# Optimization experiments

Hardware: AMD Instinct MI355X
Metric: run time of the kernel (lower is better)

## Reference

```python
import jax, jax.numpy as jnp
import numpy as np

QS, B, C, H, M = 512, 8, 1024, 16, 1536
HC = C // H
KS = QS  # xk = xv = xq (self-attention)


def setup_inputs() -> dict:
    key = jax.random.key(0)
    ks = jax.random.split(key, 16)
    scale = 1.0 / np.sqrt(C)
    xq = jax.random.normal(ks[0], (QS, B, C), jnp.float32)
    memory_kv = jax.random.normal(ks[1], (M, B, H, 2 * HC), jnp.float32)
    memory_length = jax.random.randint(ks[2], (B,), 0, M)
    pad = jax.random.randint(ks[3], (B,), 0, KS)
    mask = jnp.zeros((QS, KS, B), dtype=bool)
    Wq = jax.random.normal(ks[4], (C, C), jnp.float32) * scale
    bq = jax.random.normal(ks[5], (C,), jnp.float32) * 0.02
    Wk = jax.random.normal(ks[6], (C, C), jnp.float32) * scale
    bk = jax.random.normal(ks[7], (C,), jnp.float32) * 0.02
    Wv = jax.random.normal(ks[8], (C, C), jnp.float32) * scale
    bv = jax.random.normal(ks[9], (C,), jnp.float32) * 0.02
    Wo = jax.random.normal(ks[10], (C, C), jnp.float32) * scale
    bo = jax.random.normal(ks[11], (C,), jnp.float32) * 0.02
    return dict(xq=xq, pad=pad, mask=mask, memory_length=memory_length,
                memory_kv=memory_kv, Wq=Wq, bq=bq, Wk=Wk, bk=bk,
                Wv=Wv, bv=bv, Wo=Wo, bo=bo)


def _memory_attention(xq, pad, mask, memory_length, memory_kv,
                      Wq, bq, Wk, bk, Wv, bv, Wo, bo):
    qs, b, c = xq.shape
    m = memory_kv.shape[0]
    T = m + KS  # combined kv length (static upper bound = max(memory_length)+pad)

    # qkv projections (torch Linear: x @ W.T + b), layout (seq, batch, h, hc)
    q = (xq @ Wq.T + bq).reshape(qs, b, H, HC)
    k = (xq @ Wk.T + bk).reshape(KS, b, H, HC)
    v = (xq @ Wv.T + bv).reshape(KS, b, H, HC)

    # cat_padded_seqs as a static-shape gather: slot t of batch i is
    #   memory[t]        if t <  memory_length[i]
    #   new[t - len_i]   if t - len_i < pad[i]
    #   padding (masked) otherwise
    t = jnp.arange(T)[:, None]                      # [T,1]
    L = memory_length[None, :]                      # [1,b]
    in_mem = t < L                                  # [T,b]
    off = t - L                                     # [T,b] offset into new seq
    in_new = (off >= 0) & (off < pad[None, :])      # [T,b]
    idx_new = jnp.clip(off, 0, KS - 1)              # [T,b]

    mem_k = memory_kv[..., :HC]
    mem_v = memory_kv[..., HC:]
    mem_idx = jnp.minimum(jnp.arange(T), m - 1)     # [T]
    k_mem = mem_k[mem_idx]                          # [T,b,H,HC]
    v_mem = mem_v[mem_idx]

    gidx = jnp.broadcast_to(idx_new[:, :, None, None], (T, b, H, HC))
    k_new = jnp.take_along_axis(k, gidx, axis=0)    # [T,b,H,HC]
    v_new = jnp.take_along_axis(v, gidx, axis=0)

    sel = in_mem[:, :, None, None]
    k_comb = jnp.where(sel, k_mem, k_new)
    v_comb = jnp.where(sel, v_mem, v_new)

    # combined padding/user mask, True = masked out
    midx = jnp.broadcast_to(idx_new[None, :, :], (qs, T, b))
    user_m = jnp.take_along_axis(mask, midx, axis=1)        # [qs,T,b]
    comb_mask = jnp.where(in_mem[None], False,
                          jnp.where(in_new[None], user_m, True))

    # attention
    temperature = 1.0 / np.sqrt(HC)
    a = jnp.einsum('sbhc,tbhc->stbh', q, k_comb) * temperature
    a = jnp.where(comb_mask[:, :, :, None], -jnp.inf, a)
    p = jax.nn.softmax(a, axis=1)
    p = jnp.nan_to_num(p)  # fully-masked rows -> 0 (matches torch)
    x = jnp.einsum('stbh,tbhc->sbhc', p, v_comb).reshape(qs, b, c)
    return x @ Wo.T + bo


def reference(xq, pad, mask, memory_length, memory_kv,
              Wq, bq, Wk, bk, Wv, bv, Wo, bo):
    return _memory_attention(xq, pad, mask, memory_length, memory_kv,
                             Wq, bq, Wk, bk, Wv, bv, Wo, bo)
```

## Files before the change

### kernel.cpp

```cpp
#include <hip/hip_runtime.h>

#define QS_ 512
#define B_  8
#define C_  1024
#define H_  16
#define HC_ 64
#define M_  1536
#define KS_ 512
#define TMX 2048

typedef __attribute__((ext_vector_type(8))) short bf16x8;
typedef __attribute__((ext_vector_type(4))) float f32x4;

__device__ __forceinline__ short f2bf(float f) {
    unsigned u = __float_as_uint(f);
    unsigned r = (u + 0x7FFF + ((u >> 16) & 1)) >> 16;
    return (short)r;
}

__device__ __forceinline__ void gload_lds16(const void* g, void* l) {
    __builtin_amdgcn_global_load_lds(
        (const __attribute__((address_space(1))) unsigned int*)g,
        (__attribute__((address_space(3))) unsigned int*)l, 16, 0, 0);
}

__global__ __launch_bounds__(256) void prep_all(
    const float* __restrict__ xq,
    const float* __restrict__ w0, const float* __restrict__ w1,
    const float* __restrict__ w2, const float* __restrict__ w3,
    short* __restrict__ xqb,
    short* __restrict__ d0, short* __restrict__ d1,
    short* __restrict__ d2, short* __restrict__ d3,
    const float* __restrict__ mkv, short* __restrict__ kall,
    short* __restrict__ vall,
    const unsigned char* __restrict__ maskb, const int* __restrict__ mlen,
    const int* __restrict__ padv, unsigned char* __restrict__ mbits)
{
    __shared__ short T[64][72];
    const int bx = blockIdx.x;
    const int tid = threadIdx.x;

    if (bx < 4096) {
        int idx = bx * 256 + tid;
        const float* src; short* dst; int i;
        if (idx < 524288) { src = xq; dst = xqb; i = idx; }
        else {
            int sel = (idx >> 17) & 3;
            i = idx & 131071;
            src = sel == 0 ? w0 : sel == 1 ? w1 : sel == 2 ? w2 : w3;
            dst = sel == 0 ? d0 : sel == 1 ? d1 : sel == 2 ? d2 : d3;
        }
        const float4* s = (const float4*)src + (size_t)i * 2;
        float4 a = s[0], bq = s[1];
        short o[8];
        o[0] = f2bf(a.x);  o[1] = f2bf(a.y);  o[2] = f2bf(a.z);  o[3] = f2bf(a.w);
        o[4] = f2bf(bq.x); o[5] = f2bf(bq.y); o[6] = f2bf(bq.z); o[7] = f2bf(bq.w);
        *(uint4*)(dst + (size_t)i * 8) = *(uint4*)o;
        return;
    }

    if (bx < 7168) {
        const int idx = bx - 4096;
        const int tc = idx % 24;
        const int h  = (idx / 24) & 15;
        const int b  = idx / 384;
        const int row = tid >> 2, part = tid & 3;
        const int t = tc * 64 + row;
        const int g = b * H_ + h;
        const float4* src = (const float4*)(mkv + (((size_t)t * B_ + b) * H_ + h) * 128 + part * 32);
        short o[32];
#pragma unroll
        for (int j = 0; j < 8; ++j) {
            float4 f = src[j];
            o[j * 4 + 0] = f2bf(f.x); o[j * 4 + 1] = f2bf(f.y);
            o[j * 4 + 2] = f2bf(f.z); o[j * 4 + 3] = f2bf(f.w);
        }
        if (part < 2) {
            short* d = kall + ((size_t)g * TMX + t) * 64 + part * 32;
#pragma unroll
            for (int j = 0; j < 4; ++j) ((uint4*)d)[j] = ((uint4*)o)[j];
        } else {
            int hc0 = (part - 2) * 32;
#pragma unroll
            for (int j = 0; j < 32; ++j) T[hc0 + j][row] = o[j];
        }
        __syncthreads();
        const int hc = tid >> 2, seg = tid & 3;
        uint4 a = *(const uint4*)&T[hc][seg * 16];
        uint4 c = *(const uint4*)&T[hc][seg * 16 + 8];
        short* d = vall + ((size_t)g * HC_ + hc) * TMX + tc * 64 + seg * 16;
        ((uint4*)d)[0] = a; ((uint4*)d)[1] = c;
        return;
    }

    if (bx < 7296) {
        const int i = bx - 7168;
        const int b = i >> 4, h = i & 15;
        const int L = mlen[b], P = padv[b];
        const int te = L + P;
        const int z0 = max(1536, L + 512);
        const int z1 = min(2048, (te + 63) & ~63);
        if (z1 > z0) {
            const int g = b * 16 + h;
            const int hc = tid >> 2;
            short* rowp = vall + ((size_t)g * HC_ + hc) * TMX;
            for (int c = z0 + (tid & 3); c < z1; c += 4) rowp[c] = 0;
        }
        return;
    }

    {
        const int j = bx - 7296;
        const int b = j >> 6;
        const int q = (j & 63) * 8 + (tid >> 5);
        const int wordIdx = tid & 31;
        const int L = mlen[b], P = padv[b];
        const int tb = wordIdx * 64;
        unsigned long long w;
        if (tb + 63 < L) {
            w = 0ull;
        } else if (tb >= L + P) {
            w = ~0ull;
        } else {
            w = 0ull;
            const unsigned char* mq = maskb + (size_t)q * (KS_ * B_) + b;
#pragma unroll 4
            for (int k = 0; k < 64; ++k) {
                int t = tb + k;
                int bit;
                if (t < L) bit = 0;
                else {
                    int off = t - L;
                    bit = (off >= P) ? 1 : (mq[(size_t)off * B_] ? 1 : 0);
                }
                w |= (unsigned long long)bit << k;
            }
        }
        ((unsigned long long*)mbits)[(((size_t)(b * 512 + q)) << 5) + wordIdx] = w;
    }
}

template <bool BF16OUT, bool KSC>
__device__ __forceinline__ void gemm128_body(
    short (*As)[64], short (*Ws)[64],
    const short* __restrict__ A, const short* __restrict__ W,
    const float* __restrict__ bias, void* __restrict__ outv,
    int n0, int j0, float oscale, const int* __restrict__ mlen)
{
    const int tid  = threadIdx.x;
    const int lane = tid & 63;
    const int wave = tid >> 6;
    const int wm = (wave & 1) * 64;
    const int wn = (wave >> 1) * 64;
    const int lr = lane & 15;
    const int quad = lane >> 4;

    f32x4 acc[4][4];
#pragma unroll
    for (int i = 0; i < 4; ++i)
#pragma unroll
        for (int j = 0; j < 4; ++j)
            acc[i][j] = (f32x4){0.f, 0.f, 0.f, 0.f};

    for (int k0 = 0; k0 < C_; k0 += 64) {
#pragma unroll
        for (int p = 0; p < 4; ++p) {
            int flat = p * 256 + tid;
            int r = flat >> 3, c8 = (flat & 7) * 8;
            gload_lds16(A + (size_t)(n0 + r) * C_ + k0 + c8, (short*)As + flat * 8);
        }
#pragma unroll
        for (int p = 0; p < 4; ++p) {
            int flat = p * 256 + tid;
            int r = flat >> 3, c8 = (flat & 7) * 8;
            gload_lds16(W + (size_t)(j0 + r) * C_ + k0 + c8, (short*)Ws + flat * 8);
        }
        __syncthreads();
#pragma unroll
        for (int ks = 0; ks < 2; ++ks) {
            const int kk = ks * 32 + quad * 8;
            bf16x8 afrag[4], bfrag[4];
#pragma unroll
            for (int im = 0; im < 4; ++im)
                afrag[im] = *(const bf16x8*)&As[wm + im * 16 + lr][kk];
#pragma unroll
            for (int jn = 0; jn < 4; ++jn)
                bfrag[jn] = *(const bf16x8*)&Ws[wn + jn * 16 + lr][kk];
#pragma unroll
            for (int im = 0; im < 4; ++im)
#pragma unroll
                for (int jn = 0; jn < 4; ++jn)
                    acc[im][jn] = __builtin_amdgcn_mfma_f32_16x16x32_bf16(
                        afrag[im], bfrag[jn], acc[im][jn], 0, 0, 0);
        }
        __syncthreads();
    }

    if constexpr (KSC) {
        int ml[8];
#pragma unroll
        for (int i = 0; i < 8; ++i) ml[i] = mlen[i];
#pragma unroll
        for (int jn = 0; jn < 4; ++jn) {
            const int col = j0 + wn + jn * 16 + lr;
            const int h = col >> 6, hc = col & 63;
            const float bv = bias[col];
#pragma unroll
            for (int im = 0; im < 4; ++im) {
                const int row = n0 + wm + im * 16 + quad * 4;
#pragma unroll
                for (int r = 0; r < 4; ++r) {
                    const int rr = row + r;
                    const int s = rr >> 3, b = rr & 7;
                    float v = acc[im][jn][r] + bv;
                    ((short*)outv)[((size_t)((b * 16 + h) * TMX) + ml[b] + s) * 64 + hc] = f2bf(v);
                }
            }
        }
    } else {
#pragma unroll
        for (int jn = 0; jn < 4; ++jn) {
            const int col = j0 + wn + jn * 16 + lr;
            const float bv = bias[col];
#pragma unroll
            for (int im = 0; im < 4; ++im) {
                const int row = n0 + wm + im * 16 + quad * 4;
#pragma unroll
                for (int r = 0; r < 4; ++r) {
                    float v = (acc[im][jn][r] + bv) * oscale;
                    if (BF16OUT)
                        ((short*)outv)[(size_t)(row + r) * C_ + col] = f2bf(v);
                    else
                        ((float*)outv)[(size_t)(row + r) * C_ + col] = v;
                }
            }
        }
    }
}

template <bool BF16OUT>
__global__ __launch_bounds__(256) void gemm128(
    const short* __restrict__ A, const short* __restrict__ W,
    const float* __restrict__ bias, void* __restrict__ outv)
{
    __shared__ short As[128][64];
    __shared__ short Ws[128][64];
    gemm128_body<BF16OUT, false>(As, Ws, A, W, bias, outv,
                                 blockIdx.x * 128, blockIdx.y * 128, 1.0f, nullptr);
}

__global__ __launch_bounds__(256) void gemm128_qkv(
    const short* __restrict__ A,
    const short* __restrict__ Wq, const short* __restrict__ Wk,
    const short* __restrict__ Wv,
    const float* __restrict__ bq, const float* __restrict__ bk,
    const float* __restrict__ bv,
    short* __restrict__ oq, short* __restrict__ kall, short* __restrict__ ov,
    const int* __restrict__ mlen)
{
    __shared__ short As[128][64];
    __shared__ short Ws[128][64];
    const int sel = blockIdx.y >> 3;
    const int n0 = blockIdx.x * 128;
    const int j0 = (blockIdx.y & 7) * 128;
    if (sel == 0)
        gemm128_body<true, false>(As, Ws, A, Wq, bq, oq, n0, j0, 0.125f, nullptr);
    else if (sel == 1)
        gemm128_body<true, true>(As, Ws, A, Wk, bk, kall, n0, j0, 1.0f, mlen);
    else
        gemm128_body<true, false>(As, Ws, A, Wv, bv, ov, n0, j0, 1.0f, nullptr);
}

__global__ __launch_bounds__(256) void scatter_kv(
    const short* __restrict__ vbuf, const int* __restrict__ mlen,
    short* __restrict__ vall)
{
    __shared__ short T[64][72];
    const int bx = blockIdx.x;
    const int tid = threadIdx.x;
    const int sc = bx & 7, h = (bx >> 3) & 15, b = bx >> 7;
    const int r = tid >> 2, seg = tid & 3;
    const int s = sc * 64 + r;
    const short* src = vbuf + ((size_t)s * B_ + b) * C_ + h * HC_ + seg * 16;
    short tmp[16];
    *(uint4*)&tmp[0] = ((const uint4*)src)[0];
    *(uint4*)&tmp[8] = ((const uint4*)src)[1];
#pragma unroll
    for (int j = 0; j < 16; ++j) T[seg * 16 + j][r] = tmp[j];
    __syncthreads();
    const int L = mlen[b];
    const int hc = tid >> 2;
    const int g = b * H_ + h;
    short* drow = vall + ((size_t)g * HC_ + hc) * TMX + L + sc * 64 + seg * 16;
    const short* srow = &T[hc][seg * 16];
#pragma unroll
    for (int j = 0; j < 16; ++j) drow[j] = srow[j];
}

__global__ __launch_bounds__(256, 4) void attn_block(
    const short* __restrict__ qb, const short* __restrict__ kall,
    const short* __restrict__ vall, const unsigned char* __restrict__ mbits,
    const int* __restrict__ mlen, const int* __restrict__ padv,
    short* __restrict__ xout)
{
    __shared__ short Ks[2][64][64];
    __shared__ short Vs[2][64][64];

    const int tid  = threadIdx.x;
    const int lane = tid & 63;
    const int wave = tid >> 6;
    const int lr   = lane & 15;
    const int quad = lane >> 4;
    const int bx = blockIdx.x;
    const int g  = ((bx >> 6) << 3) | (bx & 7);
    const int qg = (bx >> 3) & 7;
    const int b  = g >> 4, h = g & 15;
    const int tend = mlen[b] + padv[b];
    const float NEG = -1e30f;

    const int q = qg * 64 + wave * 16 + lr;

    const short* qrow = qb + ((size_t)q * B_ + b) * C_ + h * HC_;
    bf16x8 q0 = *(const bf16x8*)(qrow + quad * 8);
    bf16x8 q1 = *(const bf16x8*)(qrow + 32 + quad * 8);

    const char* kg = (const char*)(kall + (size_t)g * TMX * 64);
    const char* vg = (const char*)(vall + (size_t)g * HC_ * TMX);
    const unsigned char* mrow = mbits + ((size_t)(b * 512 + q) << 8);

    f32x4 O[4];
#pragma unroll
    for (int i = 0; i < 4; ++i) O[i] = (f32x4){0.f, 0.f, 0.f, 0.f};
    float mr = NEG, lsum = 0.f;

    const int nch = (tend + 63) >> 6;

    auto stage = [&](int t0, int buf) {
        char* KsB = (char*)Ks[buf];
        char* VsB = (char*)Vs[buf];
#pragma unroll
        for (int i = 0; i < 4; ++i) {
            int p = wave * 4 + i;
            int f = ((p & 7) << 6) + lane;
            int row = f >> 3;
            int c = ((f & 7) << 4) ^ ((row & 7) << 4);
            if (p < 8)
                gload_lds16(kg + (size_t)(t0 + row) * 128 + c,
                            KsB + (size_t)f * 16);
            else
                gload_lds16(vg + (size_t)row * (TMX * 2) + (size_t)t0 * 2 + c,
                            VsB + (size_t)f * 16);
        }
    };

    if (nch > 0) stage(0, 0);
    __syncthreads();

    int cur = 0;
    for (int ci = 0; ci < nch; ++ci) {
        const int t0 = ci << 6;

        unsigned long long mw = *(const unsigned long long*)(mrow + (t0 >> 3));

        if (ci + 1 < nch) stage((ci + 1) << 6, cur ^ 1);

        const char* KsB = (const char*)Ks[cur];
        const char* VsB = (const char*)Vs[cur];

        bf16x8 kf[4][2];
#pragma unroll
        for (int tt = 0; tt < 4; ++tt) {
            int t = tt * 16 + lr;
            int sw = (t & 7) << 4;
            kf[tt][0] = *(const bf16x8*)(KsB + t * 128 + ((quad * 16) ^ sw));
            kf[tt][1] = *(const bf16x8*)(KsB + t * 128 + ((64 + quad * 16) ^ sw));
        }

        __builtin_amdgcn_s_setprio(1);
        f32x4 S[4];
#pragma unroll
        for (int tt = 0; tt < 4; ++tt) {
            f32x4 z = (f32x4){0.f, 0.f, 0.f, 0.f};
            z = __builtin_amdgcn_mfma_f32_16x16x32_bf16(kf[tt][0], q0, z, 0, 0, 0);
            S[tt] = __builtin_amdgcn_mfma_f32_16x16x32_bf16(kf[tt][1], q1, z, 0, 0, 0);
        }
        __builtin_amdgcn_s_setprio(0);

        bf16x8 vf[4][2];
#pragma unroll
        for (int ht = 0; ht < 4; ++ht) {
            int hc = ht * 16 + lr;
            int sw = (hc & 7) << 4;
            vf[ht][0] = *(const bf16x8*)(VsB + hc * 128 + ((quad * 16) ^ sw));
            vf[ht][1] = *(const bf16x8*)(VsB + hc * 128 + ((64 + quad * 16) ^ sw));
        }

        float p4[4][4];
#pragma unroll
        for (int tt = 0; tt < 4; ++tt) {
            unsigned m4 = ((unsigned)(mw >> (tt * 16 + quad * 4))) & 15u;
#pragma unroll
            for (int r = 0; r < 4; ++r)
                p4[tt][r] = (m4 & (1u << r)) ? NEG : S[tt][r];
        }

        float rm = NEG;
#pragma unroll
        for (int tt = 0; tt < 4; ++tt)
#pragma unroll
            for (int r = 0; r < 4; ++r) rm = fmaxf(rm, p4[tt][r]);
        rm = fmaxf(rm, __shfl_xor(rm, 16, 64));
        rm = fmaxf(rm, __shfl_xor(rm, 32, 64));
        const float nm = fmaxf(fmaxf(mr, rm), -1e20f);
        const float al = __expf(mr - nm);
        float rs = 0.f;
#pragma unroll
        for (int tt = 0; tt < 4; ++tt)
#pragma unroll
            for (int r = 0; r < 4; ++r) {
                float e = __expf(p4[tt][r] - nm);
                p4[tt][r] = e;
                rs += e;
            }
        rs += __shfl_xor(rs, 16, 64);
        rs += __shfl_xor(rs, 32, 64);
        lsum = lsum * al + rs;
        mr = nm;
#pragma unroll
        for (int ht = 0; ht < 4; ++ht)
#pragma unroll
            for (int r = 0; r < 4; ++r) O[ht][r] *= al;

        bf16x8 pf[2];
        const int slA = ((quad & 1) * 2) * 16 + lr;
        const int slB = slA + 16;
        const unsigned sel = (quad & 2) ? 0x07060302u : 0x05040100u;
#pragma unroll
        for (int hf = 0; hf < 2; ++hf) {
            const int tt0 = hf * 2;
            unsigned pk[4];
#pragma unroll
            for (int r = 0; r < 4; ++r) {
                unsigned o;
                asm("v_cvt_pk_bf16_f32 %0, %1, %2"
                    : "=v"(o) : "v"(p4[tt0][r]), "v"(p4[tt0 + 1][r]));
                pk[r] = o;
            }
            unsigned uA[4], uB[4];
#pragma unroll
            for (int r = 0; r < 4; ++r) {
                uA[r] = (unsigned)__shfl((int)pk[r], slA, 64);
                uB[r] = (unsigned)__shfl((int)pk[r], slB, 64);
            }
            unsigned wv[4];
            wv[0] = __builtin_amdgcn_perm(uA[1], uA[0], sel);
            wv[1] = __builtin_amdgcn_perm(uA[3], uA[2], sel);
            wv[2] = __builtin_amdgcn_perm(uB[1], uB[0], sel);
            wv[3] = __builtin_amdgcn_perm(uB[3], uB[2], sel);
            pf[hf] = *(const bf16x8*)wv;
        }

        __builtin_amdgcn_s_setprio(1);
#pragma unroll
        for (int ht = 0; ht < 4; ++ht) {
            O[ht] = __builtin_amdgcn_mfma_f32_16x16x32_bf16(vf[ht][0], pf[0], O[ht], 0, 0, 0);
            O[ht] = __builtin_amdgcn_mfma_f32_16x16x32_bf16(vf[ht][1], pf[1], O[ht], 0, 0, 0);
        }
        __builtin_amdgcn_s_setprio(0);

        __syncthreads();
        cur ^= 1;
    }

    float inv = (lsum > 0.f) ? 1.0f / lsum : 0.f;
#pragma unroll
    for (int ht = 0; ht < 4; ++ht) {
        short ov[4];
#pragma unroll
        for (int r = 0; r < 4; ++r) ov[r] = f2bf(O[ht][r] * inv);
        short* d = xout + ((size_t)q * B_ + b) * C_ + h * HC_ + ht * 16 + quad * 4;
        *(long long*)d = *(const long long*)ov;
    }
}

extern "C" void kernel_launch(void* const* d_in, const int* in_sizes, int n_in,
                              void* d_out, int out_size, void* d_ws, size_t ws_size,
                              hipStream_t stream)
{
    const float* xq   = (const float*)d_in[0];
    const int*   pad  = (const int*)d_in[1];
    const unsigned char* maskb = (const unsigned char*)d_in[2];
    const int*   mlen = (const int*)d_in[3];
    const float* mkv  = (const float*)d_in[4];
    const float* Wq   = (const float*)d_in[5];
    const float* bq   = (const float*)d_in[6];
    const float* Wk   = (const float*)d_in[7];
    const float* bk   = (const float*)d_in[8];
    const float* Wv   = (const float*)d_in[9];
    const float* bv   = (const float*)d_in[10];
    const float* Wo   = (const float*)d_in[11];
    const float* bo   = (const float*)d_in[12];
    float* out = (float*)d_out;

    short* xqb  = (short*)d_ws;
    short* wqb  = xqb  + (size_t)4194304;
    short* wkb  = wqb  + (size_t)1048576;
    short* wvb  = wkb  + (size_t)1048576;
    short* wob  = wvb  + (size_t)1048576;
    short* kall = wob  + (size_t)1048576;
    short* vall = kall + (size_t)128 * TMX * 64;
    short* qbuf = vall + (size_t)128 * HC_ * TMX;
    short* vbuf = qbuf + (size_t)4194304;
    short* xbuf = vbuf + (size_t)4194304;
    unsigned char* mbits = (unsigned char*)(xbuf + (size_t)4194304);

    dim3 gblk(256);
    prep_all<<<dim3(7808), gblk, 0, stream>>>(
        xq, Wq, Wk, Wv, Wo, xqb, wqb, wkb, wvb, wob,
        mkv, kall, vall, maskb, mlen, pad, mbits);

    gemm128_qkv<<<dim3(32, 24), gblk, 0, stream>>>(
        xqb, wqb, wkb, wvb, bq, bk, bv, qbuf, kall, vbuf, mlen);

    scatter_kv<<<dim3(1024), gblk, 0, stream>>>(vbuf, mlen, vall);

    attn_block<<<dim3(1024), gblk, 0, stream>>>(qbuf, kall, vall, mbits,
                                                mlen, pad, xbuf);

    gemm128<false><<<dim3(32, 8), gblk, 0, stream>>>(xbuf, wob, bo, out);
}
```

Baseline: 345.8 us.

## Fuse V transpose-scatter into QKV GEMM epilogue and skip unused memory rows

The QKV GEMM's V branch now writes its output directly in the transposed, memory-length-offset layout the attention kernel reads. This removes the separate scatter_kv kernel and the intermediate vbuf round trip. The prep kernel also skips converting memory_kv tiles past each batch's used length, and skips loading rows that the new K/V will overwrite. In exchange, the V epilogue issues scattered 2-byte stores with a large stride, which may coalesce poorly.

```diff
diff --git a/kernel.cpp b/kernel.cpp
--- a/kernel.cpp
+++ b/kernel.cpp
@@ -64,21 +64,32 @@
         const int tc = idx % 24;
         const int h  = (idx / 24) & 15;
         const int b  = idx / 384;
+        const int L = mlen[b];
+        const int tendb = L + padv[b];
+        if (tc * 64 >= tendb) return;
         const int row = tid >> 2, part = tid & 3;
         const int t = tc * 64 + row;
         const int g = b * H_ + h;
-        const float4* src = (const float4*)(mkv + (((size_t)t * B_ + b) * H_ + h) * 128 + part * 32);
+        const bool skiprow = (t >= L) && (t < L + 512);
         short o[32];
-#pragma unroll
-        for (int j = 0; j < 8; ++j) {
-            float4 f = src[j];
-            o[j * 4 + 0] = f2bf(f.x); o[j * 4 + 1] = f2bf(f.y);
-            o[j * 4 + 2] = f2bf(f.z); o[j * 4 + 3] = f2bf(f.w);
+        if (!skiprow) {
+            const float4* src = (const float4*)(mkv + (((size_t)t * B_ + b) * H_ + h) * 128 + part * 32);
+#pragma unroll
+            for (int j = 0; j < 8; ++j) {
+                float4 f = src[j];
+                o[j * 4 + 0] = f2bf(f.x); o[j * 4 + 1] = f2bf(f.y);
+                o[j * 4 + 2] = f2bf(f.z); o[j * 4 + 3] = f2bf(f.w);
+            }
+        } else {
+#pragma unroll
+            for (int j = 0; j < 32; ++j) o[j] = 0;
         }
         if (part < 2) {
-            short* d = kall + ((size_t)g * TMX + t) * 64 + part * 32;
-#pragma unroll
-            for (int j = 0; j < 4; ++j) ((uint4*)d)[j] = ((uint4*)o)[j];
+            if (!skiprow) {
+                short* d = kall + ((size_t)g * TMX + t) * 64 + part * 32;
+#pragma unroll
+                for (int j = 0; j < 4; ++j) ((uint4*)d)[j] = ((uint4*)o)[j];
+            }
         } else {
             int hc0 = (part - 2) * 32;
 #pragma unroll
@@ -140,7 +151,7 @@
     }
 }
 
-template <bool BF16OUT, bool KSC>
+template <int EPI>
 __device__ __forceinline__ void gemm128_body(
     short (*As)[64], short (*Ws)[64],
     const short* __restrict__ A, const short* __restrict__ W,
@@ -196,7 +207,7 @@
         __syncthreads();
     }
 
-    if constexpr (KSC) {
+    if constexpr (EPI == 2 || EPI == 3) {
         int ml[8];
 #pragma unroll
         for (int i = 0; i < 8; ++i) ml[i] = mlen[i];
@@ -213,7 +224,10 @@
                     const int rr = row + r;
                     const int s = rr >> 3, b = rr & 7;
                     float v = acc[im][jn][r] + bv;
-                    ((short*)outv)[((size_t)((b * 16 + h) * TMX) + ml[b] + s) * 64 + hc] = f2bf(v);
+                    if (EPI == 2)
+                        ((short*)outv)[((size_t)((b * 16 + h) * TMX) + ml[b] + s) * 64 + hc] = f2bf(v);
+                    else
+                        ((short*)outv)[((size_t)((b * 16 + h) * 64 + hc)) * TMX + ml[b] + s] = f2bf(v);
                 }
             }
         }
@@ -228,7 +242,7 @@
 #pragma unroll
                 for (int r = 0; r < 4; ++r) {
                     float v = (acc[im][jn][r] + bv) * oscale;
-                    if (BF16OUT)
+                    if (EPI == 1)
                         ((short*)outv)[(size_t)(row + r) * C_ + col] = f2bf(v);
                     else
                         ((float*)outv)[(size_t)(row + r) * C_ + col] = v;
@@ -238,15 +252,14 @@
     }
 }
 
-template <bool BF16OUT>
-__global__ __launch_bounds__(256) void gemm128(
+__global__ __launch_bounds__(256) void gemm128_f32(
     const short* __restrict__ A, const short* __restrict__ W,
-    const float* __restrict__ bias, void* __restrict__ outv)
+    const float* __restrict__ bias, float* __restrict__ outv)
 {
     __shared__ short As[128][64];
     __shared__ short Ws[128][64];
-    gemm128_body<BF16OUT, false>(As, Ws, A, W, bias, outv,
-                                 blockIdx.x * 128, blockIdx.y * 128, 1.0f, nullptr);
+    gemm128_body<0>(As, Ws, A, W, bias, outv,
+                    blockIdx.x * 128, blockIdx.y * 128, 1.0f, nullptr);
 }
 
 __global__ __launch_bounds__(256) void gemm128_qkv(
@@ -255,7 +268,7 @@
     const short* __restrict__ Wv,
     const float* __restrict__ bq, const float* __restrict__ bk,
     const float* __restrict__ bv,
-    short* __restrict__ oq, short* __restrict__ kall, short* __restrict__ ov,
+    short* __restrict__ oq, short* __restrict__ kall, short* __restrict__ vall,
     const int* __restrict__ mlen)
 {
     __shared__ short As[128][64];
@@ -264,37 +277,11 @@
     const int n0 = blockIdx.x * 128;
     const int j0 = (blockIdx.y & 7) * 128;
     if (sel == 0)
-        gemm128_body<true, false>(As, Ws, A, Wq, bq, oq, n0, j0, 0.125f, nullptr);
+        gemm128_body<1>(As, Ws, A, Wq, bq, oq, n0, j0, 0.125f, nullptr);
     else if (sel == 1)
-        gemm128_body<true, true>(As, Ws, A, Wk, bk, kall, n0, j0, 1.0f, mlen);
+        gemm128_body<2>(As, Ws, A, Wk, bk, kall, n0, j0, 1.0f, mlen);
     else
-        gemm128_body<true, false>(As, Ws, A, Wv, bv, ov, n0, j0, 1.0f, nullptr);
-}
-
-__global__ __launch_bounds__(256) void scatter_kv(
-    const short* __restrict__ vbuf, const int* __restrict__ mlen,
-    short* __restrict__ vall)
-{
-    __shared__ short T[64][72];
-    const int bx = blockIdx.x;
-    const int tid = threadIdx.x;
-    const int sc = bx & 7, h = (bx >> 3) & 15, b = bx >> 7;
-    const int r = tid >> 2, seg = tid & 3;
-    const int s = sc * 64 + r;
-    const short* src = vbuf + ((size_t)s * B_ + b) * C_ + h * HC_ + seg * 16;
-    short tmp[16];
-    *(uint4*)&tmp[0] = ((const uint4*)src)[0];
-    *(uint4*)&tmp[8] = ((const uint4*)src)[1];
-#pragma unroll
-    for (int j = 0; j < 16; ++j) T[seg * 16 + j][r] = tmp[j];
-    __syncthreads();
-    const int L = mlen[b];
-    const int hc = tid >> 2;
-    const int g = b * H_ + h;
-    short* drow = vall + ((size_t)g * HC_ + hc) * TMX + L + sc * 64 + seg * 16;
-    const short* srow = &T[hc][seg * 16];
-#pragma unroll
-    for (int j = 0; j < 16; ++j) drow[j] = srow[j];
+        gemm128_body<3>(As, Ws, A, Wv, bv, vall, n0, j0, 1.0f, mlen);
 }
 
 __global__ __launch_bounds__(256, 4) void attn_block(
@@ -510,8 +497,7 @@
     short* kall = wob  + (size_t)1048576;
     short* vall = kall + (size_t)128 * TMX * 64;
     short* qbuf = vall + (size_t)128 * HC_ * TMX;
-    short* vbuf = qbuf + (size_t)4194304;
-    short* xbuf = vbuf + (size_t)4194304;
+    short* xbuf = qbuf + (size_t)4194304;
     unsigned char* mbits = (unsigned char*)(xbuf + (size_t)4194304);
 
     dim3 gblk(256);
@@ -520,12 +506,10 @@
         mkv, kall, vall, maskb, mlen, pad, mbits);
 
     gemm128_qkv<<<dim3(32, 24), gblk, 0, stream>>>(
-        xqb, wqb, wkb, wvb, bq, bk, bv, qbuf, kall, vbuf, mlen);
-
-    scatter_kv<<<dim3(1024), gblk, 0, stream>>>(vbuf, mlen, vall);
+        xqb, wqb, wkb, wvb, bq, bk, bv, qbuf, kall, vall, mlen);
 
     attn_block<<<dim3(1024), gblk, 0, stream>>>(qbuf, kall, vall, mbits,
                                                 mlen, pad, xbuf);
 
-    gemm128<false><<<dim3(32, 8), gblk, 0, stream>>>(xbuf, wob, bo, out);
-}
+    gemm128_f32<<<dim3(32, 8), gblk, 0, stream>>>(xbuf, wob, bo, out);
+}
```

After: 332.9 us. 3.7% less time.
